# Kernel tuning notes

Hardware: AMD Instinct MI355X
Metric: run time of the kernel (lower is better)

## Reference

```python
import jax, jax.numpy as jnp
import numpy as np

ROPE_THETA = 10000.0

def apply_rope(x, positions):
    # x: [b, h, s, d], positions: [s]
    d = x.shape[-1]
    inv_freq = ROPE_THETA ** (-jnp.arange(0, d, 2, dtype=jnp.float32) / d)  # [d/2]
    ang = positions.astype(jnp.float32)[:, None] * inv_freq[None, :]        # [s, d/2]
    cos = jnp.cos(ang)
    sin = jnp.sin(ang)
    x1 = x[..., 0::2]
    x2 = x[..., 1::2]
    r1 = x1 * cos - x2 * sin
    r2 = x1 * sin + x2 * cos
    # interleave back to [..., d]
    return jnp.stack([r1, r2], axis=-1).reshape(x.shape)

def setup_inputs() -> dict:
    key = jax.random.key(0)
    k1, k2, k3 = jax.random.split(key, 3)
    b, s, d_model = 4, 2048, 1024
    x = jax.random.normal(k1, (b, s, d_model), dtype=jnp.float32)
    wqkv = jax.random.normal(k2, (3 * d_model, d_model), dtype=jnp.float32) * (d_model ** -0.5)
    wo = jax.random.normal(k3, (d_model, d_model), dtype=jnp.float32) * (d_model ** -0.5)
    token_positions = jnp.arange(s, dtype=jnp.int64 if jax.config.jax_enable_x64 else jnp.int32)
    return {"x": x, "wqkv": wqkv, "wo": wo, "token_positions": token_positions}

def reference(x, wqkv, wo, token_positions):
    b, s, d_model = x.shape
    num_heads = 16
    d_head = d_model // num_heads
    # fused QKV projection (Linear: y = x @ W.T)
    qkv = jnp.einsum('bse,fe->bsf', x, wqkv)  # [b, s, 3*d_model]
    q, k, v = jnp.split(qkv, 3, axis=-1)
    def to_heads(t):
        return t.reshape(b, s, num_heads, d_head).transpose(0, 2, 1, 3)  # [b, h, s, d]
    q, k, v = to_heads(q), to_heads(k), to_heads(v)
    q = apply_rope(q, token_positions)
    k = apply_rope(k, token_positions)
    scores = jnp.einsum('bhqd,bhkd->bhqk', q, k) / jnp.sqrt(jnp.asarray(d_head, dtype=x.dtype))
    causal = jnp.tril(jnp.ones((s, s), dtype=bool))  # [s, s]
    scores = jnp.where(causal, scores, -jnp.inf)
    weights = jax.nn.softmax(scores, axis=-1)
    y = jnp.einsum('bhqk,bhkd->bhqd', weights, v)
    y = y.transpose(0, 2, 1, 3).reshape(b, s, d_model)
    return jnp.einsum('bse,fe->bsf', y, wo)
```

## Files before the change

kernel.cpp:

```cpp
#include <hip/hip_runtime.h>
#include <stdint.h>


typedef __attribute__((ext_vector_type(8))) short bf16x8;
typedef __attribute__((ext_vector_type(4))) float f32x4;
typedef __attribute__((ext_vector_type(8))) unsigned short u16x8;
typedef __attribute__((ext_vector_type(4))) unsigned short u16x4;

#define NB 4
#define NS 2048
#define NH 16
#define DH 64
#define DM 1024
#define BH (NB*NH)

static __device__ __forceinline__ unsigned short f2bf(float f){
  unsigned u = __builtin_bit_cast(unsigned, f);
  u += 0x7fffu + ((u >> 16) & 1u);
  return (unsigned short)(u >> 16);
}
static __device__ __forceinline__ float bf2f(unsigned short h){
  unsigned u = ((unsigned)h) << 16;
  return __builtin_bit_cast(float, u);
}
static __device__ __forceinline__ unsigned cvt_pk_bf16(float lo, float hi){
  unsigned r;
  asm("v_cvt_pk_bf16_f32 %0, %1, %2" : "=v"(r) : "v"(lo), "v"(hi));
  return r;
}
static __device__ __forceinline__ f32x4 mfma16(bf16x8 a, bf16x8 b, f32x4 c){
  return __builtin_amdgcn_mfma_f32_16x16x32_bf16(a, b, c, 0, 0, 0);
}
static __device__ __forceinline__ void gld_lds16(const void* g, void* l){
  __builtin_amdgcn_global_load_lds((const __attribute__((address_space(1))) unsigned int*)g,
                                   (__attribute__((address_space(3))) unsigned int*)l,
                                   16, 0, 0);
}

__global__ void cvt_f32_bf16(const float* __restrict__ src,
                             unsigned short* __restrict__ dst, int n4){
  int stride = gridDim.x * blockDim.x;
  for (int i = blockIdx.x * blockDim.x + threadIdx.x; i < n4; i += stride){
    f32x4 v = *(const f32x4*)(src + (size_t)i * 4);
    u16x4 o;
    o[0] = f2bf(v[0]); o[1] = f2bf(v[1]); o[2] = f2bf(v[2]); o[3] = f2bf(v[3]);
    *(u16x4*)(dst + (size_t)i * 4) = o;
  }
}

__global__ void rope_table(const int* __restrict__ pos,
                           float* __restrict__ ct, float* __restrict__ st){
  int t = blockIdx.x * 256 + threadIdx.x;
  int s = t >> 5, i = t & 31;
  float p = (float)pos[s];
  float freq = exp2f(-(float)(2 * i) * (13.287712379549449f / 64.f));
  float a = p * freq;
  ct[t] = cosf(a);
  st[t] = sinf(a);
}

__global__ __launch_bounds__(256) void rope_qk(unsigned short* __restrict__ buf,
                                               const float* __restrict__ ct,
                                               const float* __restrict__ st){
  size_t t  = (size_t)blockIdx.x * 256 + threadIdx.x;
  size_t e0 = t * 8;
  int dh0 = (int)(e0 & 63);
  int s   = (int)((e0 >> 6) & (NS - 1));
  u16x8 v = *(const u16x8*)(buf + e0);
  f32x4 c  = *(const f32x4*)(ct + s * 32 + (dh0 >> 1));
  f32x4 sn = *(const f32x4*)(st + s * 32 + (dh0 >> 1));
  u16x8 o;
#pragma unroll
  for (int i = 0; i < 4; i++){
    float x1 = bf2f(v[2*i]), x2 = bf2f(v[2*i+1]);
    o[2*i]   = f2bf(x1 * c[i] - x2 * sn[i]);
    o[2*i+1] = f2bf(x1 * sn[i] + x2 * c[i]);
  }
  *(u16x8*)(buf + e0) = o;
}

template<int BM, int BN, int MF, int NFR, int EPI>
__global__ __launch_bounds__((BM/(MF*16))*(BN/(NFR*16))*64, 2)
void gemm_ring(const unsigned short* __restrict__ A,
               const unsigned short* __restrict__ Bm,
               void* __restrict__ out0, void* __restrict__ out1,
               void* __restrict__ out2, int M, int N, int K){
  constexpr int WM = BM / (MF * 16);
  constexpr int WN = BN / (NFR * 16);
  constexpr int T  = WM * WN * 64;
  constexpr int LA = BM * 4 / T;
  constexpr int LB = BN * 4 / T;
  __shared__ __attribute__((aligned(16))) unsigned short As[4][BM * 32];
  __shared__ __attribute__((aligned(16))) unsigned short Bs[4][BN * 32];
  int tid = threadIdx.x;
  int w = tid >> 6, l = tid & 63;
  int lr = l & 15, lk = l >> 4;
  int m0 = blockIdx.y * BM, n0 = blockIdx.x * BN;
  int wr = (w / WN) * (MF * 16), wc = (w % WN) * (NFR * 16);

  const int nt = K >> 5;

  auto stage = [&](int t, int buf){
    int k0 = t * 32;
#pragma unroll
    for (int i = 0; i < LA; i++){
      int f = i * T + tid;
      int row = f >> 2, c = f & 3;
      int gc = (c ^ ((row >> 1) & 3)) * 8;
      gld_lds16(A + (size_t)(m0 + row) * K + k0 + gc, &As[buf][(i * T + w * 64) * 8]);
    }
#pragma unroll
    for (int i = 0; i < LB; i++){
      int f = i * T + tid;
      int row = f >> 2, c = f & 3;
      int gc = (c ^ ((row >> 1) & 3)) * 8;
      gld_lds16(Bm + (size_t)(n0 + row) * K + k0 + gc, &Bs[buf][(i * T + w * 64) * 8]);
    }
  };

  f32x4 zero = {0.f, 0.f, 0.f, 0.f};
  f32x4 acc[MF][NFR];
#pragma unroll
  for (int a = 0; a < MF; a++)
#pragma unroll
    for (int b = 0; b < NFR; b++) acc[a][b] = zero;

  stage(0, 0); stage(1, 1); stage(2, 2);
  asm volatile("s_waitcnt vmcnt(%0)" :: "i"(2 * (LA + LB)) : "memory");
  __builtin_amdgcn_sched_barrier(0);
  __builtin_amdgcn_s_barrier();
  __builtin_amdgcn_sched_barrier(0);

  for (int t = 0; t < nt; ++t){
    int buf = t & 3;
    bf16x8 af[MF], bfr[NFR];
#pragma unroll
    for (int mf = 0; mf < MF; mf++){
      int row = wr + mf * 16 + lr;
      af[mf] = *(const bf16x8*)&As[buf][row * 32 + ((lk ^ ((row >> 1) & 3)) * 8)];
    }
#pragma unroll
    for (int nf = 0; nf < NFR; nf++){
      int row = wc + nf * 16 + lr;
      bfr[nf] = *(const bf16x8*)&Bs[buf][row * 32 + ((lk ^ ((row >> 1) & 3)) * 8)];
    }
    if (t + 3 < nt) stage(t + 3, (t + 3) & 3);
    __builtin_amdgcn_s_setprio(1);
#pragma unroll
    for (int mf = 0; mf < MF; mf++)
#pragma unroll
      for (int nf = 0; nf < NFR; nf++)
        acc[mf][nf] = mfma16(af[mf], bfr[nf], acc[mf][nf]);
    __builtin_amdgcn_s_setprio(0);
    if (t + 3 < nt)      { asm volatile("s_waitcnt vmcnt(%0)" :: "i"(2 * (LA + LB)) : "memory"); }
    else if (t + 2 < nt) { asm volatile("s_waitcnt vmcnt(%0)" :: "i"(LA + LB) : "memory"); }
    else if (t + 1 < nt) { asm volatile("s_waitcnt vmcnt(0)" ::: "memory"); }
    __builtin_amdgcn_sched_barrier(0);
    __builtin_amdgcn_s_barrier();
    __builtin_amdgcn_sched_barrier(0);
  }

  if (EPI == 0){
    unsigned short* q  = (unsigned short*)out0;
    unsigned short* k  = (unsigned short*)out1;
    unsigned short* vt = (unsigned short*)out2;
#pragma unroll
    for (int mf = 0; mf < MF; mf++)
#pragma unroll
      for (int nf = 0; nf < NFR; nf++)
#pragma unroll
        for (int j = 0; j < 4; j++){
          int m = m0 + wr + mf * 16 + lk * 4 + j;
          int n = n0 + wc + nf * 16 + lr;
          int part = n >> 10, c = n & 1023;
          int h = c >> 6, dh = c & 63;
          int b = m >> 11, s = m & (NS - 1);
          unsigned short val = f2bf(acc[mf][nf][j]);
          if (part == 2){
            vt[((size_t)((b * NH + h) * DH + dh)) * NS + s] = val;
          } else {
            size_t off = ((size_t)(b * NH + h) * NS + s) * DH + dh;
            ((part == 0) ? q : k)[off] = val;
          }
        }
  } else {
    float* C = (float*)out0;
#pragma unroll
    for (int mf = 0; mf < MF; mf++)
#pragma unroll
      for (int nf = 0; nf < NFR; nf++)
#pragma unroll
        for (int j = 0; j < 4; j++){
          int m = m0 + wr + mf * 16 + lk * 4 + j;
          int n = n0 + wc + nf * 16 + lr;
          C[(size_t)m * N + n] = acc[mf][nf][j];
        }
  }
}

__global__ __launch_bounds__(256, 3) void fa_kernel(const unsigned short* __restrict__ qb_,
                                                    const unsigned short* __restrict__ kbuf,
                                                    const unsigned short* __restrict__ vtb,
                                                    unsigned short* __restrict__ yb){
  __shared__ __attribute__((aligned(16))) unsigned short Kl[2][4096];
  __shared__ __attribute__((aligned(16))) unsigned short Vl[2][4096];
  __shared__ __attribute__((aligned(16))) unsigned short Pl[4][32 * 76];
  int tid = threadIdx.x;
  int w = tid >> 6, l = tid & 63;
  int lr = l & 15, lk = l >> 4;
  int qb = 15 - blockIdx.y;
  int bh = blockIdx.x;
  int b = bh >> 4, h = bh & 15;
  int qr0 = qb * 128 + w * 32;
  const unsigned short* Q  = qb_  + (size_t)bh * NS * DH;
  const unsigned short* Kp = kbuf + (size_t)bh * NS * DH;
  const unsigned short* VT = vtb  + (size_t)bh * DH * NS;
  unsigned short* Pw = &Pl[w][0];

  int r8  = l >> 3;
  int swc = ((l & 7) ^ (r8 & 7)) * 8;

  auto stage = [&](int buf, int t){
    int kbase = t * 64;
    if (w < 2){
#pragma unroll
      for (int ii = 0; ii < 4; ii++){
        int i = w * 4 + ii;
        gld_lds16(Kp + (size_t)(kbase + i * 8 + r8) * DH + swc, &Kl[buf][i * 512]);
      }
    } else {
#pragma unroll
      for (int ii = 0; ii < 4; ii++){
        int i = (w - 2) * 4 + ii;
        gld_lds16(VT + (size_t)(i * 8 + r8) * NS + kbase + swc, &Vl[buf][i * 512]);
      }
    }
  };

  bf16x8 qf[2][2];
#pragma unroll
  for (int mf = 0; mf < 2; mf++)
#pragma unroll
    for (int ks = 0; ks < 2; ks++)
      qf[mf][ks] = *(const bf16x8*)(Q + (size_t)(qr0 + mf * 16 + lr) * DH + ks * 32 + lk * 8);

  f32x4 zero = {0.f, 0.f, 0.f, 0.f};
  f32x4 O[2][4];
  float lsum[2];
#pragma unroll
  for (int mf = 0; mf < 2; mf++){
#pragma unroll
    for (int nf = 0; nf < 4; nf++) O[mf][nf] = zero;
    lsum[mf] = 0.f;
  }

  const float SC = 0.18033688011112042f;
  const int ntile = 2 * qb + 2;

  stage(0, 0);
  __syncthreads();

  int cur = 0;
  for (int t = 0; t < ntile; ++t){
    int kbase = t * 64;
    if (t + 1 < ntile) stage(cur ^ 1, t + 1);

    if (kbase <= qr0 + 31){
      bf16x8 kf[4][2];
#pragma unroll
      for (int nf = 0; nf < 4; nf++){
        int row = nf * 16 + lr;
        int ro = row * 64, sw = (row & 7) << 3;
#pragma unroll
        for (int ks = 0; ks < 2; ks++)
          kf[nf][ks] = *(const bf16x8*)&Kl[cur][ro + ((ks * 32 + lk * 8) ^ sw)];
      }
      bf16x8 vf[2][4];
#pragma unroll
      for (int nfd = 0; nfd < 4; nfd++){
        int row = nfd * 16 + lr;
        int ro = row * 64, sw = (row & 7) << 3;
#pragma unroll
        for (int ks = 0; ks < 2; ks++)
          vf[ks][nfd] = *(const bf16x8*)&Vl[cur][ro + ((ks * 32 + lk * 8) ^ sw)];
      }

      f32x4 sa[2][4];
#pragma unroll
      for (int mf = 0; mf < 2; mf++)
#pragma unroll
        for (int nf = 0; nf < 4; nf++) sa[mf][nf] = zero;
#pragma unroll
      for (int nf = 0; nf < 4; nf++)
#pragma unroll
        for (int mf = 0; mf < 2; mf++){
          sa[mf][nf] = mfma16(kf[nf][0], qf[mf][0], sa[mf][nf]);
          sa[mf][nf] = mfma16(kf[nf][1], qf[mf][1], sa[mf][nf]);
        }

      bool domask = (kbase + 63 > qr0);

#pragma unroll
      for (int mf = 0; mf < 2; mf++){
        int qg = qr0 + mf * 16 + lr;
        float ls = 0.f;
#pragma unroll
        for (int nf = 0; nf < 4; nf++){
          float p4[4];
#pragma unroll
          for (int j = 0; j < 4; j++){
            float xx = __builtin_fmaf(sa[mf][nf][j], SC, -8.0f);
            if (domask){
              int kg = kbase + nf * 16 + lk * 4 + j;
              if (kg > qg) xx = -__builtin_inff();
            }
            float p = exp2f(xx);
            ls += p;
            p4[j] = p;
          }
          unsigned d0 = cvt_pk_bf16(p4[0], p4[1]);
          unsigned d1 = cvt_pk_bf16(p4[2], p4[3]);
          int base = (mf * 16 + lr) * 76 + nf * 16 + lk * 4;
          *(unsigned*)&Pw[base]     = d0;
          *(unsigned*)&Pw[base + 2] = d1;
        }
        lsum[mf] += ls;
      }

      bf16x8 pf[2][2];
#pragma unroll
      for (int mf = 0; mf < 2; mf++)
#pragma unroll
        for (int ks = 0; ks < 2; ks++)
          pf[mf][ks] = *(const bf16x8*)&Pw[(mf * 16 + lr) * 76 + ks * 32 + lk * 8];
#pragma unroll
      for (int ks = 0; ks < 2; ks++)
#pragma unroll
        for (int nfd = 0; nfd < 4; nfd++)
#pragma unroll
          for (int mf = 0; mf < 2; mf++)
            O[mf][nfd] = mfma16(pf[mf][ks], vf[ks][nfd], O[mf][nfd]);
    }

    __syncthreads();
    cur ^= 1;
  }

#pragma unroll
  for (int mf = 0; mf < 2; mf++){
    lsum[mf] += __shfl_xor(lsum[mf], 16);
    lsum[mf] += __shfl_xor(lsum[mf], 32);
  }
#pragma unroll
  for (int mf = 0; mf < 2; mf++)
#pragma unroll
    for (int j = 0; j < 4; j++){
      float s = __shfl(lsum[mf], lk * 4 + j);
      float inv = 1.0f / s;
      int srow = qr0 + mf * 16 + lk * 4 + j;
      unsigned short* yp = yb + ((size_t)(b * NS + srow)) * DM + h * DH;
#pragma unroll
      for (int nfd = 0; nfd < 4; nfd++)
        yp[nfd * 16 + lr] = f2bf(O[mf][nfd][j] * inv);
    }
}

extern "C" void kernel_launch(void* const* d_in, const int* in_sizes, int n_in,
                              void* d_out, int out_size, void* d_ws, size_t ws_size,
                              hipStream_t stream){
  const float* x    = (const float*)d_in[0];
  const float* wqkv = (const float*)d_in[1];
  const float* wo   = (const float*)d_in[2];
  const int*   pos  = (const int*)d_in[3];
  float* out = (float*)d_out;

  char* ws = (char*)d_ws;
  size_t off = 0;
  auto alloc = [&](size_t bytes) -> void* {
    void* p = ws + off;
    off += (bytes + 255) & ~(size_t)255;
    return p;
  };
  const size_t NE = (size_t)BH * NS * DH;
  unsigned short* xb    = (unsigned short*)alloc((size_t)8192 * 1024 * 2);
  unsigned short* wqkvb = (unsigned short*)alloc((size_t)3072 * 1024 * 2);
  unsigned short* wob   = (unsigned short*)alloc((size_t)1024 * 1024 * 2);
  unsigned short* q  = (unsigned short*)alloc(NE * 2);
  unsigned short* k  = (unsigned short*)alloc(NE * 2);
  unsigned short* vt = (unsigned short*)alloc(NE * 2);
  unsigned short* y  = (unsigned short*)alloc(NE * 2);
  float* ct = (float*)alloc((size_t)NS * 32 * 4);
  float* st = (float*)alloc((size_t)NS * 32 * 4);

  cvt_f32_bf16<<<2048, 256, 0, stream>>>(x,    xb,    8192 * 1024 / 4);
  cvt_f32_bf16<<<2048, 256, 0, stream>>>(wqkv, wqkvb, 3072 * 1024 / 4);
  cvt_f32_bf16<<<1024, 256, 0, stream>>>(wo,   wob,   1024 * 1024 / 4);
  rope_table<<<256, 256, 0, stream>>>(pos, ct, st);
  gemm_ring<128, 128, 4, 4, 0><<<dim3(24, 64), 256, 0, stream>>>(
      xb, wqkvb, q, k, vt, 8192, 3072, 1024);
  rope_qk<<<4096, 256, 0, stream>>>(q, ct, st);
  rope_qk<<<4096, 256, 0, stream>>>(k, ct, st);
  fa_kernel<<<dim3(64, 16), 256, 0, stream>>>(q, k, vt, y);
  gemm_ring<128, 128, 4, 4, 1><<<dim3(8, 64), 256, 0, stream>>>(
      y, wob, out, nullptr, nullptr, 8192, 1024, 1024);
}
```

Baseline: 223.7 us.

## Fuse RoPE into QKV GEMM epilogue, merge conversions, remap blocks per XCD

RoPE is now applied inside the QKV GEMM epilogue. Each lane exchanges its pair element with its neighbour via a lane shuffle and reads the cos/sin tables directly, so the two standalone rope passes over q and k are removed. The three f32-to-bf16 conversion launches are merged into one kernel. GEMM block indices are remapped so that consecutive M-tiles land on the same XCD, which is meant to improve L2 reuse. Costs are extra table loads and branches in the epilogue, plus per-element branching in the conversion kernel.

Measured after the change: 229.9 us. 1.03x slower.

```diff
diff --git a/kernel.cpp b/kernel.cpp
--- a/kernel.cpp
+++ b/kernel.cpp
@@ -37,14 +37,22 @@
                                    16, 0, 0);
 }
 
-__global__ void cvt_f32_bf16(const float* __restrict__ src,
-                             unsigned short* __restrict__ dst, int n4){
+__global__ __launch_bounds__(256) void cvt_all(const float* __restrict__ x,
+                                               const float* __restrict__ wqkv,
+                                               const float* __restrict__ wo,
+                                               unsigned short* __restrict__ xb,
+                                               unsigned short* __restrict__ wqkvb,
+                                               unsigned short* __restrict__ wob){
   int stride = gridDim.x * blockDim.x;
-  for (int i = blockIdx.x * blockDim.x + threadIdx.x; i < n4; i += stride){
-    f32x4 v = *(const f32x4*)(src + (size_t)i * 4);
+  for (int i = blockIdx.x * blockDim.x + threadIdx.x; i < 3145728; i += stride){
+    const float* src; unsigned short* dst; int j;
+    if (i < 2097152){ src = x; dst = xb; j = i; }
+    else if (i < 2883584){ src = wqkv; dst = wqkvb; j = i - 2097152; }
+    else { src = wo; dst = wob; j = i - 2883584; }
+    f32x4 v = *(const f32x4*)(src + (size_t)j * 4);
     u16x4 o;
     o[0] = f2bf(v[0]); o[1] = f2bf(v[1]); o[2] = f2bf(v[2]); o[3] = f2bf(v[3]);
-    *(u16x4*)(dst + (size_t)i * 4) = o;
+    *(u16x4*)(dst + (size_t)j * 4) = o;
   }
 }
 
@@ -59,32 +67,14 @@
   st[t] = sinf(a);
 }
 
-__global__ __launch_bounds__(256) void rope_qk(unsigned short* __restrict__ buf,
-                                               const float* __restrict__ ct,
-                                               const float* __restrict__ st){
-  size_t t  = (size_t)blockIdx.x * 256 + threadIdx.x;
-  size_t e0 = t * 8;
-  int dh0 = (int)(e0 & 63);
-  int s   = (int)((e0 >> 6) & (NS - 1));
-  u16x8 v = *(const u16x8*)(buf + e0);
-  f32x4 c  = *(const f32x4*)(ct + s * 32 + (dh0 >> 1));
-  f32x4 sn = *(const f32x4*)(st + s * 32 + (dh0 >> 1));
-  u16x8 o;
-#pragma unroll
-  for (int i = 0; i < 4; i++){
-    float x1 = bf2f(v[2*i]), x2 = bf2f(v[2*i+1]);
-    o[2*i]   = f2bf(x1 * c[i] - x2 * sn[i]);
-    o[2*i+1] = f2bf(x1 * sn[i] + x2 * c[i]);
-  }
-  *(u16x8*)(buf + e0) = o;
-}
-
 template<int BM, int BN, int MF, int NFR, int EPI>
 __global__ __launch_bounds__((BM/(MF*16))*(BN/(NFR*16))*64, 2)
 void gemm_ring(const unsigned short* __restrict__ A,
                const unsigned short* __restrict__ Bm,
                void* __restrict__ out0, void* __restrict__ out1,
-               void* __restrict__ out2, int M, int N, int K){
+               void* __restrict__ out2,
+               const float* __restrict__ ct, const float* __restrict__ st,
+               int M, int N, int K){
   constexpr int WM = BM / (MF * 16);
   constexpr int WN = BN / (NFR * 16);
   constexpr int T  = WM * WN * 64;
@@ -95,7 +85,13 @@
   int tid = threadIdx.x;
   int w = tid >> 6, l = tid & 63;
   int lr = l & 15, lk = l >> 4;
-  int m0 = blockIdx.y * BM, n0 = blockIdx.x * BN;
+
+  int o = blockIdx.y * gridDim.x + blockIdx.x;
+  int xcd = o & 7, t8 = o >> 3;
+  int mpx = gridDim.y >> 3;
+  int by = xcd * mpx + t8 / gridDim.x;
+  int bx = t8 % gridDim.x;
+  int m0 = by * BM, n0 = bx * BN;
   int wr = (w / WN) * (MF * 16), wc = (w % WN) * (NFR * 16);
 
   const int nt = K >> 5;
@@ -175,12 +171,17 @@
           int part = n >> 10, c = n & 1023;
           int h = c >> 6, dh = c & 63;
           int b = m >> 11, s = m & (NS - 1);
-          unsigned short val = f2bf(acc[mf][nf][j]);
+          float val = acc[mf][nf][j];
+          float other = __shfl_xor(val, 1);
           if (part == 2){
-            vt[((size_t)((b * NH + h) * DH + dh)) * NS + s] = val;
+            vt[((size_t)((b * NH + h) * DH + dh)) * NS + s] = f2bf(val);
           } else {
+            int ti = s * 32 + (dh >> 1);
+            float cc = ct[ti], sn = st[ti];
+            float r = (dh & 1) ? (other * sn + val * cc)
+                               : (val * cc - other * sn);
             size_t off = ((size_t)(b * NH + h) * NS + s) * DH + dh;
-            ((part == 0) ? q : k)[off] = val;
+            ((part == 0) ? q : k)[off] = f2bf(r);
           }
         }
   } else {
@@ -392,15 +393,11 @@
   float* ct = (float*)alloc((size_t)NS * 32 * 4);
   float* st = (float*)alloc((size_t)NS * 32 * 4);
 
-  cvt_f32_bf16<<<2048, 256, 0, stream>>>(x,    xb,    8192 * 1024 / 4);
-  cvt_f32_bf16<<<2048, 256, 0, stream>>>(wqkv, wqkvb, 3072 * 1024 / 4);
-  cvt_f32_bf16<<<1024, 256, 0, stream>>>(wo,   wob,   1024 * 1024 / 4);
+  cvt_all<<<3072, 256, 0, stream>>>(x, wqkv, wo, xb, wqkvb, wob);
   rope_table<<<256, 256, 0, stream>>>(pos, ct, st);
   gemm_ring<128, 128, 4, 4, 0><<<dim3(24, 64), 256, 0, stream>>>(
-      xb, wqkvb, q, k, vt, 8192, 3072, 1024);
-  rope_qk<<<4096, 256, 0, stream>>>(q, ct, st);
-  rope_qk<<<4096, 256, 0, stream>>>(k, ct, st);
+      xb, wqkvb, q, k, vt, ct, st, 8192, 3072, 1024);
   fa_kernel<<<dim3(64, 16), 256, 0, stream>>>(q, k, vt, y);
   gemm_ring<128, 128, 4, 4, 1><<<dim3(8, 64), 256, 0, stream>>>(
-      y, wob, out, nullptr, nullptr, 8192, 1024, 1024);
-}
+      y, wob, out, nullptr, nullptr, nullptr, nullptr, 8192, 1024, 1024);
+}
```
